# Kernel tuning notes

Hardware: AMD Instinct MI355X
Metric: run time of the kernel (lower is better)

The kernel has to match this reference:

```python
import jax, jax.numpy as jnp
import numpy as np

B, T, N, H = 16, 49, 64, 128  # batch, input_window_size-1, nbones, hidden_size


def setup_inputs() -> dict:
    key = jax.random.key(0)
    ks = jax.random.split(key, 13)
    s = 0.1  # keep gate preactivations in a sane range
    inp = {
        "h": jax.random.normal(ks[0], (B, T, N, H), jnp.float32),
        "c_h": jax.random.normal(ks[1], (B, T, N, H), jnp.float32),
        "p": jax.random.normal(ks[2], (B, T, N, H), jnp.float32),
        "g_t": jax.random.normal(ks[3], (B, T, 1, H), jnp.float32),
        "c_g_t": jax.random.normal(ks[4], (B, T, 1, H), jnp.float32),
        # 8 h-update gates stacked: order = (i, f_lt, f_ft, f_rt, f_s, g, o, c)
        "U": jax.random.normal(ks[5], (8, T, H, H), jnp.float32) * s,     # acts on p
        "Wt": jax.random.normal(ks[6], (8, T, 3 * H, H), jnp.float32) * s,  # acts on [h_before,h,h_after]
        "Ws": jax.random.normal(ks[7], (8, T, H, H), jnp.float32) * s,    # acts on h_s_before
        "Zt": jax.random.normal(ks[8], (8, T, H, H), jnp.float32) * s,    # acts on g_t
        "b": jax.random.normal(ks[9], (8, T, 1, H), jnp.float32) * s,
        # 3 g_t-update gates stacked: order = (forget_f, g, o)
        "Wg": jax.random.normal(ks[10], (3, T, H, H), jnp.float32) * s,
        "Zg": jax.random.normal(ks[11], (3, T, H, H), jnp.float32) * s,
        "bg": jax.random.normal(ks[12], (3, T, 1, H), jnp.float32) * s,
        "train": 0,
    }
    return inp


def _forward(h, c_h, p, g_t, c_g_t, U, Wt, Ws, Zt, b, Wg, Zg, bg):
    zt = jnp.zeros_like(h[:, :1])        # temporal padding [B,1,N,H]
    zs = jnp.zeros_like(h[:, :, :1])     # spatial  padding [B,T,1,H]
    h_tb = jnp.concatenate([zt, h[:, :-1]], axis=1)
    h_ta = jnp.concatenate([h[:, 1:], zt], axis=1)
    h_tba = jnp.concatenate([h_tb, h, h_ta], axis=3)   # [B,T,N,3H]
    c_tb = jnp.concatenate([zt, c_h[:, :-1]], axis=1)
    c_ta = jnp.concatenate([c_h[:, 1:], zt], axis=1)
    h_sb = jnp.concatenate([zs, h[:, :, :-1]], axis=2)
    c_sb = jnp.concatenate([zs, c_h[:, :, :-1]], axis=2)

    # all 8 gate preactivations at once; per-timestep weights contracted with einsum
    pre = (jnp.einsum('btnh,gthk->gbtnk', p, U)
           + jnp.einsum('btnd,gtdk->gbtnk', h_tba, Wt)
           + jnp.einsum('btnh,gthk->gbtnk', h_sb, Ws)
           + jnp.einsum('btoh,gthk->gbtok', g_t, Zt)   # o == 1, broadcasts over bones
           + b[:, None])                               # [8,B,T,N,H]
    i_n, f_lt, f_ft, f_rt, f_s, g_n, o_n = jax.nn.sigmoid(pre[:7])
    c_n = jnp.tanh(pre[7])

    c_h_new = (i_n * c_n + f_lt * c_tb + f_ft * c_h + f_rt * c_ta
               + f_s * c_sb + g_n * c_g_t)
    h_new = o_n * jnp.tanh(c_h_new)

    # global (g_t) state update
    h_mean = jnp.mean(h_new, axis=2, keepdims=True)    # [B,T,1,H]
    f_gtf = jax.nn.sigmoid(jnp.einsum('btnh,thk->btnk', h_new, Wg[0])
                           + jnp.einsum('btoh,thk->btok', g_t, Zg[0]) + bg[0])
    g_gtg = jax.nn.sigmoid(jnp.einsum('btoh,thk->btok', h_mean, Wg[1])
                           + jnp.einsum('btoh,thk->btok', g_t, Zg[1]) + bg[1])
    o_gto = jax.nn.sigmoid(jnp.einsum('btoh,thk->btok', h_mean, Wg[2])
                           + jnp.einsum('btoh,thk->btok', g_t, Zg[2]) + bg[2])
    c_g_new = jnp.mean(f_gtf * c_h_new, axis=2, keepdims=True) + g_gtg * c_g_t
    g_new = jnp.tanh(c_g_new) * o_gto
    return h_new, c_h_new, g_new, c_g_new


def reference(h, c_h, p, g_t, c_g_t, U, Wt, Ws, Zt, b, Wg, Zg, bg, train):
    return _forward(h, c_h, p, g_t, c_g_t, U, Wt, Ws, Zt, b, Wg, Zg, bg)
```

## Files before the change

kernel.cpp:

```cpp
#include <hip/hip_runtime.h>
#include <hip/hip_bf16.h>

#define TD 49
#define BD 16
#define ND 64
#define HD 128

typedef float  f32x4  __attribute__((ext_vector_type(4)));
typedef __bf16 bf16x8 __attribute__((ext_vector_type(8)));
typedef __bf16 bf16x4 __attribute__((ext_vector_type(4)));

#define WP_OFF   0u
#define WP_ELEMS 38535168u
#define HB_OFF   38535168u
#define ACT_ELEMS 6422528u
#define PB_OFF   44957696u
#define GB_OFF   51380224u
#define GT_ELEMS 100352u
#define ZP_OFF   51480576u

#define OUT_H    0
#define OUT_CH   6422528
#define OUT_G    12845056
#define OUT_CG   12945408

#define KPAD 136
#define LDS1_BYTES 131072

__device__ __forceinline__ float sigf(float x) {
    return 1.0f / (1.0f + exp2f(-1.442695041f * x));
}
__device__ __forceinline__ float tanhf_fast(float x) {
    x = fminf(fmaxf(x, -20.f), 20.f);
    float e = exp2f(2.885390082f * x);
    return (e - 1.f) / (e + 1.f);
}
__device__ __forceinline__ void gload16(const void* g, void* l) {
    __builtin_amdgcn_global_load_lds((const __attribute__((address_space(1))) void*)g,
                                     (__attribute__((address_space(3))) void*)l, 16, 0, 0);
}

__global__ void prep_acts(const float* __restrict__ h, const float* __restrict__ p,
                          const float* __restrict__ g, __bf16* __restrict__ ws)
{
    unsigned i = blockIdx.x * 256u + threadIdx.x;
    const unsigned HU = ACT_ELEMS / 4u, GU = GT_ELEMS / 4u;
    const float* src;
    unsigned dst;
    if (i < HU)                 { src = h + (size_t)i * 4;          dst = HB_OFF + i * 4; }
    else if (i < 2u*HU)         { unsigned j = i - HU;   src = p + (size_t)j * 4; dst = PB_OFF + j * 4; }
    else if (i < 2u*HU + GU)    { unsigned j = i - 2u*HU; src = g + (size_t)j * 4; dst = GB_OFF + j * 4; }
    else if (i < 2u*HU + GU + 512u) {
        unsigned j = i - 2u*HU - GU;
        bf16x4 z = {};
        *(bf16x4*)(ws + ZP_OFF + j * 4) = z;
        return;
    } else return;
    f32x4 v = *(const f32x4*)src;
    bf16x4 w;
    w[0] = (__bf16)v[0]; w[1] = (__bf16)v[1]; w[2] = (__bf16)v[2]; w[3] = (__bf16)v[3];
    *(bf16x4*)(ws + dst) = w;
}

__global__ __launch_bounds__(256) void prep_w(
    const float* __restrict__ U, const float* __restrict__ Wt,
    const float* __restrict__ Ws, const float* __restrict__ Zt,
    __bf16* __restrict__ wp)
{
    __shared__ __bf16 tile[64 * 132];
    int bid = blockIdx.x;
    int tg  = bid / 12;
    int c   = bid % 12;
    int t   = tg >> 3, g = tg & 7;
    int gt  = g * TD + t;
    int tid = threadIdx.x;
    int k0  = c * 64;

#pragma unroll
    for (int u = 0; u < 8; ++u) {
        int unit = u * 256 + tid;
        int kk = unit >> 5;
        int h4 = (unit & 31) << 2;
        int k  = k0 + kk;
        const float* src;
        if (k < 128)      src = U  + ((size_t)(gt * 128 + k)       << 7);
        else if (k < 512) src = Wt + ((size_t)(gt * 384 + (k-128)) << 7);
        else if (k < 640) src = Ws + ((size_t)(gt * 128 + (k-512)) << 7);
        else              src = Zt + ((size_t)(gt * 128 + (k-640)) << 7);
        f32x4 v = *(const f32x4*)(src + h4);
        bf16x4 w;
        w[0] = (__bf16)v[0]; w[1] = (__bf16)v[1]; w[2] = (__bf16)v[2]; w[3] = (__bf16)v[3];
        *(bf16x4*)(tile + kk * 132 + h4) = w;
    }
    __syncthreads();
#pragma unroll
    for (int u = 0; u < 2; ++u) {
        int unit = u * 256 + tid;
        int hh = unit >> 2;
        int kg = unit & 3;
        bf16x8 v0, v1;
#pragma unroll
        for (int j = 0; j < 8; ++j) v0[j] = tile[(kg * 16 + j) * 132 + hh];
#pragma unroll
        for (int j = 0; j < 8; ++j) v1[j] = tile[(kg * 16 + 8 + j) * 132 + hh];
        __bf16* dst = wp + (size_t)(tg * 128 + hh) * 768 + k0 + kg * 16;
        *(bf16x8*)dst       = v0;
        *(bf16x8*)(dst + 8) = v1;
    }
}

__global__ __launch_bounds__(512, 1) void phase1_kernel(
    const __bf16* __restrict__ ws,
    const float* __restrict__ c_h, const float* __restrict__ c_g_t,
    const float* __restrict__ bias, float* __restrict__ out)
{
    extern __shared__ __bf16 smem[];
    const __bf16* hb = ws + HB_OFF;
    const __bf16* pb = ws + PB_OFF;
    const __bf16* gb = ws + GB_OFF;
    const __bf16* wp = ws + WP_OFF;
    const __bf16* zp = ws + ZP_OFF;

    int bid = blockIdx.x;
    int swz = (bid & 7) * 98 + (bid >> 3);
    int t     = swz >> 4;
    int rem   = swz & 15;
    int mtile = rem >> 2, ntile = rem & 3;

    int tid  = threadIdx.x;
    int wave = tid >> 6, lane = tid & 63;
    int wm = wave >> 1, wh = wave & 1;
    int lg = lane >> 4, l16 = lane & 15;

    const int R0   = (wave << 3) + (lane >> 3);
    const int k16s = ((lane & 7) ^ (R0 & 7)) << 3;
    const int n    = R0;

    f32x4 acc[4][8];
    const f32x4 vzero = {0.f, 0.f, 0.f, 0.f};
#pragma unroll
    for (int mi = 0; mi < 4; ++mi)
#pragma unroll
        for (int g = 0; g < 8; ++g) acc[mi][g] = vzero;

    int rbA[4], rsA[4], rbB[8], rsB[8];
#pragma unroll
    for (int mi = 0; mi < 4; ++mi) {
        int row = wm * 64 + mi * 16 + l16;
        rbA[mi] = row << 7;
        rsA[mi] = (row & 7) << 4;
    }
#pragma unroll
    for (int g = 0; g < 8; ++g) {
        int row = g * 32 + wh * 16 + l16;
        rbB[g] = row << 7;
        rsB[g] = (row & 7) << 4;
    }
    const int kb0 = lg << 4;

#define STAGE_A(BUF, KS) do {                                                   \
        int s_   = (KS) >> 1;                                                   \
        int koff = (((KS) & 1) << 6) + k16s;                                    \
        _Pragma("unroll")                                                       \
        for (int it = 0; it < 4; ++it) {                                        \
            int b_  = mtile * 4 + it;                                           \
            int bt_ = b_ * TD + t;                                              \
            const __bf16* src;                                                  \
            if (s_ == 0)      src = pb + ((bt_ * ND + n) << 7) + koff;          \
            else if (s_ == 1) src = (t > 0)    ? hb + (((bt_-1) * ND + n) << 7) + koff : zp; \
            else if (s_ == 2) src = hb + ((bt_ * ND + n) << 7) + koff;          \
            else if (s_ == 3) src = (t < TD-1) ? hb + (((bt_+1) * ND + n) << 7) + koff : zp; \
            else if (s_ == 4) src = (n > 0)    ? hb + ((bt_ * ND + n - 1) << 7) + koff : zp; \
            else              src = gb + (bt_ << 7) + koff;                     \
            __bf16* dst = smem + (BUF) * 16384 + (wave + it * 8) * 512;         \
            gload16(src, dst);                                                  \
        }                                                                       \
    } while (0)

#define STAGE_B(BUF, KS) do {                                                   \
        _Pragma("unroll")                                                       \
        for (int it = 0; it < 4; ++it) {                                        \
            int np = R0 + it * 64;                                              \
            int g_ = np >> 5, hc = np & 31;                                     \
            const __bf16* src = wp + (size_t)((t * 8 + g_) * 128 + ntile * 32 + hc) * 768 \
                                   + ((KS) << 6) + k16s;                        \
            __bf16* dst = smem + 32768 + (BUF) * 16384 + (wave + it * 8) * 512; \
            gload16(src, dst);                                                  \
        }                                                                       \
    } while (0)

    STAGE_A(0, 0);
    STAGE_B(0, 0);
    __syncthreads();

    int buf = 0;
    for (int ks = 0; ks < 12; ++ks) {
        if (ks < 11) {
            STAGE_A(buf ^ 1, ks + 1);
            STAGE_B(buf ^ 1, ks + 1);
        }
        const char* Ab = (const char*)(smem + buf * 16384);
        const char* Bb = (const char*)(smem + 32768 + buf * 16384);
#pragma unroll
        for (int ks32 = 0; ks32 < 2; ++ks32) {
            bf16x8 af[4], bfr[8];
#pragma unroll
            for (int mi = 0; mi < 4; ++mi)
                af[mi] = *(const bf16x8*)(Ab + rbA[mi] + (((ks32 << 6) + kb0) ^ rsA[mi]));
#pragma unroll
            for (int g = 0; g < 8; ++g)
                bfr[g] = *(const bf16x8*)(Bb + rbB[g] + (((ks32 << 6) + kb0) ^ rsB[g]));
#pragma unroll
            for (int mi = 0; mi < 4; ++mi)
#pragma unroll
                for (int g = 0; g < 8; ++g)
                    acc[mi][g] = __builtin_amdgcn_mfma_f32_16x16x32_bf16(af[mi], bfr[g], acc[mi][g], 0, 0, 0);
        }
        __syncthreads();
        buf ^= 1;
    }

    const int hcol = ntile * 32 + wh * 16 + l16;
    float bv[8];
#pragma unroll
    for (int g = 0; g < 8; ++g) bv[g] = bias[(g * TD + t) * HD + hcol];

#pragma unroll
    for (int mi = 0; mi < 4; ++mi) {
#pragma unroll
        for (int r = 0; r < 4; ++r) {
            int RG = mtile * 256 + wm * 64 + mi * 16 + lg * 4 + r;
            int b  = RG >> 6, nn = RG & 63;
            int bt = b * TD + t;
            int base = ((bt * ND + nn) << 7) + hcol;
            float pre[8];
#pragma unroll
            for (int g = 0; g < 8; ++g) pre[g] = acc[mi][g][r] + bv[g];
            float i_  = sigf(pre[0]);
            float flt = sigf(pre[1]);
            float fft = sigf(pre[2]);
            float frt = sigf(pre[3]);
            float fs  = sigf(pre[4]);
            float gn  = sigf(pre[5]);
            float on  = sigf(pre[6]);
            float cn  = tanhf_fast(pre[7]);
            float ccur = c_h[base];
            float ctb  = (t > 0)      ? c_h[base - ND * HD] : 0.f;
            float cta  = (t < TD - 1) ? c_h[base + ND * HD] : 0.f;
            float csb  = (nn > 0)     ? c_h[base - HD]      : 0.f;
            float cg   = c_g_t[(bt << 7) + hcol];
            float cnew = i_ * cn + flt * ctb + fft * ccur + frt * cta + fs * csb + gn * cg;
            float hnew = on * tanhf_fast(cnew);
            out[OUT_H  + base] = hnew;
            out[OUT_CH + base] = cnew;
        }
    }
#undef STAGE_A
#undef STAGE_B
}

__global__ __launch_bounds__(256, 2) void phase2_kernel(
    const float* __restrict__ g_t, const float* __restrict__ c_g_t,
    const float* __restrict__ Wg,  const float* __restrict__ Zg,
    const float* __restrict__ bg,  float* __restrict__ out)
{
    __shared__ __bf16 A2[64 * KPAD];
    __shared__ __bf16 Wb[128 * KPAD];
    __shared__ float  gts[128];
    __shared__ float  hm[128];
    __shared__ float  dots[5][128];
    __shared__ float  ps[2][128];
    __shared__ float  red[4][128];

    const int bid  = blockIdx.x;
    const int t    = bid >> 4;
    const int b    = bid & 15;
    const int tid  = threadIdx.x;
    const int wv   = tid >> 6;
    const int lane = tid & 63;
    const int lg   = lane >> 4;
    const int l16  = lane & 15;
    const int bt   = b * TD + t;

    const float* hn  = out + OUT_H;
    const float* chn = out + OUT_CH;

#pragma unroll
    for (int j = 0; j < 8; ++j) {
        int fid = j * 256 + tid;
        int r   = fid >> 5;
        int k   = (fid & 31) << 2;
        f32x4 v = *(const f32x4*)(hn + ((bt * ND + r) << 7) + k);
        bf16x4 w;
        w[0] = (__bf16)v[0]; w[1] = (__bf16)v[1]; w[2] = (__bf16)v[2]; w[3] = (__bf16)v[3];
        *(bf16x4*)(A2 + r * KPAD + k) = w;
    }
    if (tid < 128) gts[tid] = g_t[(bt << 7) + tid];
    __syncthreads();

    {
        int c = tid & 127, half = tid >> 7;
        float sum_ = 0.f;
        for (int r2 = 0; r2 < 32; ++r2) sum_ += (float)A2[(half * 32 + r2) * KPAD + c];
        ps[half][c] = sum_;
    }
    __syncthreads();
    if (tid < 128) hm[tid] = (ps[0][tid] + ps[1][tid]) * (1.f / 64.f);

    for (int m = 0; m < 5; ++m) {
        const float* M = (m < 3) ? (Zg + ((size_t)(m * TD + t) << 14))
                                 : (Wg + ((size_t)((m - 2) * TD + t) << 14));
        const bool use_hm = (m >= 3);
        __syncthreads();
#pragma unroll
        for (int j = 0; j < 16; ++j) {
            int fid = j * 256 + tid;
            int k   = fid >> 5;
            int c4  = (fid & 31) << 2;
            f32x4 v = *(const f32x4*)(M + (k << 7) + c4);
            bf16x4 w;
            w[0] = (__bf16)v[0]; w[1] = (__bf16)v[1]; w[2] = (__bf16)v[2]; w[3] = (__bf16)v[3];
            *(bf16x4*)(Wb + (k << 7) + c4) = w;
        }
        __syncthreads();
        {
            int c = tid & 127, half = tid >> 7;
            const float* vec = use_hm ? hm : gts;
            float sum_ = 0.f;
            for (int k = half * 64; k < half * 64 + 64; ++k)
                sum_ += vec[k] * (float)Wb[(k << 7) + c];
            ps[half][c] = sum_;
        }
        __syncthreads();
        if (tid < 128) dots[m][tid] = ps[0][tid] + ps[1][tid];
    }

    {
        const float* M = Wg + ((size_t)t << 14);
        __syncthreads();
#pragma unroll
        for (int j = 0; j < 16; ++j) {
            int fid = j * 256 + tid;
            int k   = fid >> 5;
            int q   = fid & 31;
            f32x4 v = *(const f32x4*)(M + (k << 7) + q * 4);
            int cb = q * 4;
            Wb[(cb + 0) * KPAD + k] = (__bf16)v[0];
            Wb[(cb + 1) * KPAD + k] = (__bf16)v[1];
            Wb[(cb + 2) * KPAD + k] = (__bf16)v[2];
            Wb[(cb + 3) * KPAD + k] = (__bf16)v[3];
        }
        __syncthreads();
    }

    f32x4 acc[8];
    const f32x4 vzero = {0.f, 0.f, 0.f, 0.f};
#pragma unroll
    for (int cf = 0; cf < 8; ++cf) acc[cf] = vzero;
#pragma unroll
    for (int ks = 0; ks < 4; ++ks) {
        int kb = ks * 32 + lg * 8;
        bf16x8 a = *(const bf16x8*)(A2 + (wv * 16 + l16) * KPAD + kb);
#pragma unroll
        for (int cf = 0; cf < 8; ++cf) {
            bf16x8 bfr = *(const bf16x8*)(Wb + (cf * 16 + l16) * KPAD + kb);
            acc[cf] = __builtin_amdgcn_mfma_f32_16x16x32_bf16(a, bfr, acc[cf], 0, 0, 0);
        }
    }

#pragma unroll
    for (int cf = 0; cf < 8; ++cf) {
        int col = cf * 16 + l16;
        float z = dots[0][col] + bg[(0 * TD + t) * HD + col];
        float macc = 0.f;
#pragma unroll
        for (int r = 0; r < 4; ++r) {
            int row = wv * 16 + lg * 4 + r;
            float f  = sigf(acc[cf][r] + z);
            float cv = chn[((bt * ND + row) << 7) + col];
            macc += f * cv;
        }
        macc += __shfl_xor(macc, 16, 64);
        macc += __shfl_xor(macc, 32, 64);
        if (lane < 16) red[wv][col] = macc;
    }
    __syncthreads();
    if (tid < 128) {
        int c = tid;
        float Mn  = (red[0][c] + red[1][c] + red[2][c] + red[3][c]) * (1.f / 64.f);
        float g_g = sigf(dots[3][c] + dots[1][c] + bg[(1 * TD + t) * HD + c]);
        float o_g = sigf(dots[4][c] + dots[2][c] + bg[(2 * TD + t) * HD + c]);
        float cgt = c_g_t[(bt << 7) + c];
        float cgn = Mn + g_g * cgt;
        float gnw = tanhf_fast(cgn) * o_g;
        out[OUT_G  + (bt << 7) + c] = gnw;
        out[OUT_CG + (bt << 7) + c] = cgn;
    }
}

extern "C" void kernel_launch(void* const* d_in, const int* in_sizes, int n_in,
                              void* d_out, int out_size, void* d_ws, size_t ws_size,
                              hipStream_t stream) {
    const float* h     = (const float*)d_in[0];
    const float* c_h   = (const float*)d_in[1];
    const float* p     = (const float*)d_in[2];
    const float* g_t   = (const float*)d_in[3];
    const float* c_g_t = (const float*)d_in[4];
    const float* U     = (const float*)d_in[5];
    const float* Wt    = (const float*)d_in[6];
    const float* Ws    = (const float*)d_in[7];
    const float* Zt    = (const float*)d_in[8];
    const float* b     = (const float*)d_in[9];
    const float* Wg    = (const float*)d_in[10];
    const float* Zg    = (const float*)d_in[11];
    const float* bg    = (const float*)d_in[12];
    float* out = (float*)d_out;
    __bf16* ws = (__bf16*)d_ws;

    prep_acts<<<12644, 256, 0, stream>>>(h, p, g_t, ws);
    prep_w<<<TD * 8 * 12, 256, 0, stream>>>(U, Wt, Ws, Zt, ws + WP_OFF);

    (void)hipFuncSetAttribute(reinterpret_cast<const void*>(phase1_kernel),
                              hipFuncAttributeMaxDynamicSharedMemorySize, LDS1_BYTES);
    phase1_kernel<<<TD * 16, 512, LDS1_BYTES, stream>>>(ws, c_h, c_g_t, b, out);
    phase2_kernel<<<TD * BD, 256, 0, stream>>>(g_t, c_g_t, Wg, Zg, bg, out);
}
```

Before: 257.8 us.

## Deepen GEMM K-loop pipeline with two-ahead prefetch and split LDS/MFMA phases

Restructures the K loop so two stages are in flight. Each iteration first reads all LDS fragments for the current step into registers and waits on them, then passes a barrier. It then issues the global-to-LDS loads for step ks+2 into the same buffer and runs the MFMAs at raised priority. Explicit vmcnt waits replace __syncthreads, so global loads can overlap compute further ahead. The cost is a doubled fragment register footprint, and correctness now depends on the hand-set vmcnt counts matching the number of issued loads.

```diff
diff --git a/kernel.cpp b/kernel.cpp
--- a/kernel.cpp
+++ b/kernel.cpp
@@ -191,33 +191,56 @@
 
     STAGE_A(0, 0);
     STAGE_B(0, 0);
-    __syncthreads();
-
-    int buf = 0;
+    STAGE_A(1, 1);
+    STAGE_B(1, 1);
+    asm volatile("s_waitcnt vmcnt(8)" ::: "memory");
+    __builtin_amdgcn_sched_barrier(0);
+    __builtin_amdgcn_s_barrier();
+
     for (int ks = 0; ks < 12; ++ks) {
-        if (ks < 11) {
-            STAGE_A(buf ^ 1, ks + 1);
-            STAGE_B(buf ^ 1, ks + 1);
-        }
+        const int buf = ks & 1;
         const char* Ab = (const char*)(smem + buf * 16384);
         const char* Bb = (const char*)(smem + 32768 + buf * 16384);
+
+        bf16x8 af[2][4], bfr[2][8];
 #pragma unroll
         for (int ks32 = 0; ks32 < 2; ++ks32) {
-            bf16x8 af[4], bfr[8];
 #pragma unroll
             for (int mi = 0; mi < 4; ++mi)
-                af[mi] = *(const bf16x8*)(Ab + rbA[mi] + (((ks32 << 6) + kb0) ^ rsA[mi]));
+                af[ks32][mi] = *(const bf16x8*)(Ab + rbA[mi] + (((ks32 << 6) + kb0) ^ rsA[mi]));
 #pragma unroll
             for (int g = 0; g < 8; ++g)
-                bfr[g] = *(const bf16x8*)(Bb + rbB[g] + (((ks32 << 6) + kb0) ^ rsB[g]));
+                bfr[ks32][g] = *(const bf16x8*)(Bb + rbB[g] + (((ks32 << 6) + kb0) ^ rsB[g]));
+        }
+        asm volatile("s_waitcnt lgkmcnt(0)" ::: "memory");
+        __builtin_amdgcn_sched_barrier(0);
+        __builtin_amdgcn_s_barrier();
+
+        if (ks + 2 < 12) {
+            STAGE_A(buf, ks + 2);
+            STAGE_B(buf, ks + 2);
+        }
+        __builtin_amdgcn_sched_barrier(0);
+
+        __builtin_amdgcn_s_setprio(1);
+#pragma unroll
+        for (int ks32 = 0; ks32 < 2; ++ks32)
 #pragma unroll
             for (int mi = 0; mi < 4; ++mi)
 #pragma unroll
                 for (int g = 0; g < 8; ++g)
-                    acc[mi][g] = __builtin_amdgcn_mfma_f32_16x16x32_bf16(af[mi], bfr[g], acc[mi][g], 0, 0, 0);
-        }
-        __syncthreads();
-        buf ^= 1;
+                    acc[mi][g] = __builtin_amdgcn_mfma_f32_16x16x32_bf16(af[ks32][mi], bfr[ks32][g], acc[mi][g], 0, 0, 0);
+        __builtin_amdgcn_s_setprio(0);
+
+        if (ks < 11) {
+            if (ks + 2 < 12) {
+                asm volatile("s_waitcnt vmcnt(8)" ::: "memory");
+            } else {
+                asm volatile("s_waitcnt vmcnt(0)" ::: "memory");
+            }
+            __builtin_amdgcn_sched_barrier(0);
+            __builtin_amdgcn_s_barrier();
+        }
     }
 
     const int hcol = ntile * 32 + wh * 16 + l16;
```

Measured after the change: 303.5 us. 17.7% more time.

## Shrink phase1 GEMM tile to 128x128 with 256 threads and two blocks per CU

Applied to the files above, without the earlier changes.

Each phase1 block now covers a 128-row by 16-column (times 8 gates) output tile with 4 waves instead of 256 rows by 32 columns with 8 waves. The grid grows from 784 to 3136 blocks, LDS per block halves to 64 KB, and launch bounds allow two blocks per CU. A and B staging are merged into one loop. The aim is better occupancy and load balance across the 256 CUs, but smaller tiles give less data reuse per loaded byte and more global traffic for weights and activations.

```diff
diff --git a/kernel.cpp b/kernel.cpp
--- a/kernel.cpp
+++ b/kernel.cpp
@@ -25,7 +25,7 @@
 #define OUT_CG   12945408
 
 #define KPAD 136
-#define LDS1_BYTES 131072
+#define LDS1_BYTES 65536
 
 __device__ __forceinline__ float sigf(float x) {
     return 1.0f / (1.0f + exp2f(-1.442695041f * x));
@@ -109,7 +109,7 @@
     }
 }
 
-__global__ __launch_bounds__(512, 1) void phase1_kernel(
+__global__ __launch_bounds__(256, 2) void phase1_kernel(
     const __bf16* __restrict__ ws,
     const float* __restrict__ c_h, const float* __restrict__ c_g_t,
     const float* __restrict__ bias, float* __restrict__ out)
@@ -122,96 +122,84 @@
     const __bf16* zp = ws + ZP_OFF;
 
     int bid = blockIdx.x;
-    int swz = (bid & 7) * 98 + (bid >> 3);
-    int t     = swz >> 4;
-    int rem   = swz & 15;
-    int mtile = rem >> 2, ntile = rem & 3;
+    int swz = (bid & 7) * 392 + (bid >> 3);
+    int t     = swz >> 6;
+    int rem   = swz & 63;
+    int mtile = rem >> 3, ntile = rem & 7;
 
     int tid  = threadIdx.x;
     int wave = tid >> 6, lane = tid & 63;
-    int wm = wave >> 1, wh = wave & 1;
     int lg = lane >> 4, l16 = lane & 15;
 
-    const int R0   = (wave << 3) + (lane >> 3);
-    const int k16s = ((lane & 7) ^ (R0 & 7)) << 3;
-    const int n    = R0;
-
-    f32x4 acc[4][8];
+    const int ls   = lane >> 3;
+    const int k16s = ((lane & 7) ^ ls) << 3;
+
+    f32x4 acc[2][8];
     const f32x4 vzero = {0.f, 0.f, 0.f, 0.f};
 #pragma unroll
-    for (int mi = 0; mi < 4; ++mi)
+    for (int mi = 0; mi < 2; ++mi)
 #pragma unroll
         for (int g = 0; g < 8; ++g) acc[mi][g] = vzero;
 
-    int rbA[4], rsA[4], rbB[8], rsB[8];
-#pragma unroll
-    for (int mi = 0; mi < 4; ++mi) {
-        int row = wm * 64 + mi * 16 + l16;
+    int rbA[2], rsA[2], rbB[8], rsB[8];
+#pragma unroll
+    for (int mi = 0; mi < 2; ++mi) {
+        int row = wave * 32 + mi * 16 + l16;
         rbA[mi] = row << 7;
         rsA[mi] = (row & 7) << 4;
     }
 #pragma unroll
     for (int g = 0; g < 8; ++g) {
-        int row = g * 32 + wh * 16 + l16;
+        int row = g * 16 + l16;
         rbB[g] = row << 7;
-        rsB[g] = (row & 7) << 4;
+        rsB[g] = (l16 & 7) << 4;
     }
     const int kb0 = lg << 4;
 
-#define STAGE_A(BUF, KS) do {                                                   \
+#define STAGE(BUF, KS) do {                                                     \
         int s_   = (KS) >> 1;                                                   \
         int koff = (((KS) & 1) << 6) + k16s;                                    \
         _Pragma("unroll")                                                       \
         for (int it = 0; it < 4; ++it) {                                        \
-            int b_  = mtile * 4 + it;                                           \
+            int chunk = it * 4 + wave;                                          \
+            int R   = chunk * 8 + ls;                                           \
+            int b_  = mtile * 2 + (R >> 6);                                     \
+            int n_  = R & 63;                                                   \
             int bt_ = b_ * TD + t;                                              \
-            const __bf16* src;                                                  \
-            if (s_ == 0)      src = pb + ((bt_ * ND + n) << 7) + koff;          \
-            else if (s_ == 1) src = (t > 0)    ? hb + (((bt_-1) * ND + n) << 7) + koff : zp; \
-            else if (s_ == 2) src = hb + ((bt_ * ND + n) << 7) + koff;          \
-            else if (s_ == 3) src = (t < TD-1) ? hb + (((bt_+1) * ND + n) << 7) + koff : zp; \
-            else if (s_ == 4) src = (n > 0)    ? hb + ((bt_ * ND + n - 1) << 7) + koff : zp; \
-            else              src = gb + (bt_ << 7) + koff;                     \
-            __bf16* dst = smem + (BUF) * 16384 + (wave + it * 8) * 512;         \
-            gload16(src, dst);                                                  \
+            const __bf16* srcA;                                                 \
+            if (s_ == 0)      srcA = pb + ((bt_ * ND + n_) << 7) + koff;        \
+            else if (s_ == 1) srcA = (t > 0)    ? hb + (((bt_-1) * ND + n_) << 7) + koff : zp; \
+            else if (s_ == 2) srcA = hb + ((bt_ * ND + n_) << 7) + koff;        \
+            else if (s_ == 3) srcA = (t < TD-1) ? hb + (((bt_+1) * ND + n_) << 7) + koff : zp; \
+            else if (s_ == 4) srcA = (n_ > 0)   ? hb + ((bt_ * ND + n_ - 1) << 7) + koff : zp; \
+            else              srcA = gb + (bt_ << 7) + koff;                    \
+            gload16(srcA, smem + (BUF) * 8192 + chunk * 512);                   \
+            int g_ = R >> 4, hc = R & 15;                                       \
+            const __bf16* srcB = wp + (size_t)((t * 8 + g_) * 128 + ntile * 16 + hc) * 768 \
+                                    + ((KS) << 6) + k16s;                       \
+            gload16(srcB, smem + 16384 + (BUF) * 8192 + chunk * 512);           \
         }                                                                       \
     } while (0)
 
-#define STAGE_B(BUF, KS) do {                                                   \
-        _Pragma("unroll")                                                       \
-        for (int it = 0; it < 4; ++it) {                                        \
-            int np = R0 + it * 64;                                              \
-            int g_ = np >> 5, hc = np & 31;                                     \
-            const __bf16* src = wp + (size_t)((t * 8 + g_) * 128 + ntile * 32 + hc) * 768 \
-                                   + ((KS) << 6) + k16s;                        \
-            __bf16* dst = smem + 32768 + (BUF) * 16384 + (wave + it * 8) * 512; \
-            gload16(src, dst);                                                  \
-        }                                                                       \
-    } while (0)
-
-    STAGE_A(0, 0);
-    STAGE_B(0, 0);
+    STAGE(0, 0);
     __syncthreads();
 
     int buf = 0;
     for (int ks = 0; ks < 12; ++ks) {
-        if (ks < 11) {
-            STAGE_A(buf ^ 1, ks + 1);
-            STAGE_B(buf ^ 1, ks + 1);
-        }
-        const char* Ab = (const char*)(smem + buf * 16384);
-        const char* Bb = (const char*)(smem + 32768 + buf * 16384);
+        if (ks < 11) STAGE(buf ^ 1, ks + 1);
+        const char* Ab = (const char*)(smem + buf * 8192);
+        const char* Bb = (const char*)(smem + 16384 + buf * 8192);
 #pragma unroll
         for (int ks32 = 0; ks32 < 2; ++ks32) {
-            bf16x8 af[4], bfr[8];
-#pragma unroll
-            for (int mi = 0; mi < 4; ++mi)
+            bf16x8 af[2], bfr[8];
+#pragma unroll
+            for (int mi = 0; mi < 2; ++mi)
                 af[mi] = *(const bf16x8*)(Ab + rbA[mi] + (((ks32 << 6) + kb0) ^ rsA[mi]));
 #pragma unroll
             for (int g = 0; g < 8; ++g)
                 bfr[g] = *(const bf16x8*)(Bb + rbB[g] + (((ks32 << 6) + kb0) ^ rsB[g]));
 #pragma unroll
-            for (int mi = 0; mi < 4; ++mi)
+            for (int mi = 0; mi < 2; ++mi)
 #pragma unroll
                 for (int g = 0; g < 8; ++g)
                     acc[mi][g] = __builtin_amdgcn_mfma_f32_16x16x32_bf16(af[mi], bfr[g], acc[mi][g], 0, 0, 0);
@@ -220,16 +208,16 @@
         buf ^= 1;
     }
 
-    const int hcol = ntile * 32 + wh * 16 + l16;
+    const int hcol = ntile * 16 + l16;
     float bv[8];
 #pragma unroll
     for (int g = 0; g < 8; ++g) bv[g] = bias[(g * TD + t) * HD + hcol];
 
 #pragma unroll
-    for (int mi = 0; mi < 4; ++mi) {
+    for (int mi = 0; mi < 2; ++mi) {
 #pragma unroll
         for (int r = 0; r < 4; ++r) {
-            int RG = mtile * 256 + wm * 64 + mi * 16 + lg * 4 + r;
+            int RG = mtile * 128 + wave * 32 + mi * 16 + lg * 4 + r;
             int b  = RG >> 6, nn = RG & 63;
             int bt = b * TD + t;
             int base = ((bt * ND + nn) << 7) + hcol;
@@ -255,8 +243,7 @@
             out[OUT_CH + base] = cnew;
         }
     }
-#undef STAGE_A
-#undef STAGE_B
+#undef STAGE
 }
 
 __global__ __launch_bounds__(256, 2) void phase2_kernel(
@@ -422,6 +409,6 @@
 
     (void)hipFuncSetAttribute(reinterpret_cast<const void*>(phase1_kernel),
                               hipFuncAttributeMaxDynamicSharedMemorySize, LDS1_BYTES);
-    phase1_kernel<<<TD * 16, 512, LDS1_BYTES, stream>>>(ws, c_h, c_g_t, b, out);
+    phase1_kernel<<<TD * 64, 256, LDS1_BYTES, stream>>>(ws, c_h, c_g_t, b, out);
     phase2_kernel<<<TD * BD, 256, 0, stream>>>(g_t, c_g_t, Wg, Zg, bg, out);
 }
```

Result: no change. 253.3 us (-1.8%).
